# Optimization experiments

Hardware: AMD Instinct MI355X
Metric: run time of the kernel (lower is better)

Reference implementation:

```python
import jax, jax.numpy as jnp
import numpy as np
from jax import lax

B, L, D, F = 32, 512, 256, 256
K = 3
EPS = 1e-5


def _layer_norm(h, g, b):
    mu = jnp.mean(h, axis=-1, keepdims=True)
    var = jnp.var(h, axis=-1, keepdims=True)
    return (h - mu) * lax.rsqrt(var + EPS) * g + b


def _conv1d(h, w, b):
    # h: [B, L, Cin], w: [K, Cin, Cout] -> [B, L, Cout], 'same' padding (pad=1, k=3)
    return lax.conv_general_dilated(h, w, window_strides=(1,), padding=[(1, 1)],
                                    dimension_numbers=('NWC', 'WIO', 'NWC')) + b


def _duration_predictor(x, c1w, c1b, ln1g, ln1b, c2w, c2b, ln2g, ln2b, lw, lb):
    h = jax.nn.relu(_layer_norm(_conv1d(x, c1w, c1b), ln1g, ln1b))
    h = jax.nn.relu(_layer_norm(_conv1d(h, c2w, c2b), ln2g, ln2b))
    d = jax.nn.relu(h @ lw + lb)  # [B, L, 1]
    return d[..., 0]              # [B, L] (squeeze, training mode)


def _expand_one(xb, dur, M):
    # xb: [L, D], dur: [L] int. Repeat row i dur[i] times, zero-pad to M frames.
    cs = jnp.cumsum(dur)                              # [L]
    t = jnp.arange(M)                                 # [M]
    idx = jnp.searchsorted(cs, t, side='right')       # phoneme id per frame
    valid = t < cs[-1]
    out = jnp.take(xb, jnp.clip(idx, 0, xb.shape[0] - 1), axis=0)
    return jnp.where(valid[:, None], out, jnp.zeros((), xb.dtype))


def setup_inputs() -> dict:
    key = jax.random.key(0)
    ks = jax.random.split(key, 8)
    s_c = 1.0 / np.sqrt(K * F)
    s_l = 1.0 / np.sqrt(F)
    return {
        'x': jax.random.normal(ks[0], (B, L, D), jnp.float32),
        'durations': jax.random.randint(ks[1], (B, L), 0, 7),
        'mel_max_length': 4096,
        'conv1_w': jax.random.normal(ks[2], (K, D, F), jnp.float32) * s_c,
        'conv1_b': jnp.zeros((F,), jnp.float32),
        'ln1_g': jnp.ones((F,), jnp.float32),
        'ln1_b': jnp.zeros((F,), jnp.float32),
        'conv2_w': jax.random.normal(ks[3], (K, F, F), jnp.float32) * s_c,
        'conv2_b': jnp.zeros((F,), jnp.float32),
        'ln2_g': jnp.ones((F,), jnp.float32),
        'ln2_b': jnp.zeros((F,), jnp.float32),
        'lin_w': jax.random.normal(ks[4], (F, 1), jnp.float32) * s_l,
        'lin_b': jnp.zeros((1,), jnp.float32),
    }


def reference(x, durations, mel_max_length, conv1_w, conv1_b, ln1_g, ln1_b,
              conv2_w, conv2_b, ln2_g, ln2_b, lin_w, lin_b):
    dur_pred = _duration_predictor(x, conv1_w, conv1_b, ln1_g, ln1_b,
                                   conv2_w, conv2_b, ln2_g, ln2_b, lin_w, lin_b)
    dur = durations.astype(jnp.int32)
    output = jax.vmap(lambda xb, db: _expand_one(xb, db, mel_max_length))(x, dur)
    return output, dur_pred
```

## Files before the change

### kernel.cpp

```cpp
#include <hip/hip_runtime.h>

typedef __attribute__((ext_vector_type(8))) short short8;
typedef __attribute__((ext_vector_type(4))) float f32x4;

#define BATCH 32
#define LSEQ  512
#define DIN   256
#define FDIM  256
#define KTOT  768
#define MT    32
#define BK    32
#define PADA  264

__device__ __forceinline__ short f2bf(float f) {
    union { float f; unsigned u; } v; v.f = f;
    unsigned r = v.u + 0x7FFFu + ((v.u >> 16) & 1u);
    return (short)(r >> 16);
}

__global__ __launch_bounds__(512)
void prep_kernel(const int* __restrict__ dur, int* __restrict__ fidx, int M,
                 const float* __restrict__ w1, const float* __restrict__ w2,
                 short* __restrict__ wt1, short* __restrict__ wt2) {
    __shared__ int s[LSEQ];
    const int t = threadIdx.x, b = blockIdx.x;
    if (b < BATCH) {
        s[t] = dur[b * LSEQ + t];
        __syncthreads();
        for (int off = 1; off < LSEQ; off <<= 1) {
            int v = (t >= off) ? s[t - off] : 0;
            __syncthreads();
            s[t] += v;
            __syncthreads();
        }
        for (int f = t; f < M; f += 512) fidx[b * M + f] = -1;
        __syncthreads();
        int lo = (t == 0) ? 0 : s[t - 1];
        int hi = s[t];
        if (hi > M) hi = M;
        for (int j = lo; j < hi; j++) fidx[b * M + j] = b * LSEQ + t;
    } else {
        const int id = (b - BATCH) * 512 + t;
        const int n = id & 255, k = id >> 8;
        const int dst = (((k >> 5) * FDIM) + n) * BK + (k & 31);
        wt1[dst] = f2bf(w1[id]);
        wt2[dst] = f2bf(w2[id]);
    }
}

template<bool AF32, bool FUSE>
__global__ __launch_bounds__(256)
void conv_ln(const void* __restrict__ Asrc, const short* __restrict__ Bt,
             const float* __restrict__ cb, const float* __restrict__ g,
             const float* __restrict__ bta, const float* __restrict__ lw,
             const float* __restrict__ lb, short* __restrict__ Hout,
             float* __restrict__ Dout)
{
    __shared__ short As[34][PADA];
    __shared__ float redS[MT][4];
    __shared__ float redQ[MT][4];
    __shared__ float redD[MT][4];
    __shared__ float muS[MT];
    __shared__ float rsS[MT];

    const int tid  = threadIdx.x;
    const int wave = tid >> 6;
    const int lane = tid & 63;
    const int ml   = lane & 15;
    const int q    = lane >> 4;
    const int row0 = blockIdx.x * MT;
    const int bb   = row0 >> 9;
    const int r0   = row0 & (LSEQ - 1);

    for (int idx = tid; idx < 34 * 32; idx += 256) {
        const int r = idx >> 5, part = idx & 31;
        const int l2 = r0 + r - 1;
        short8 v = {0, 0, 0, 0, 0, 0, 0, 0};
        if (l2 >= 0 && l2 < LSEQ) {
            const size_t off = ((size_t)(bb * LSEQ + l2)) * DIN + part * 8;
            if (AF32) {
                const float4* s4 = (const float4*)((const float*)Asrc + off);
                float4 u0 = s4[0], u1 = s4[1];
                v[0] = f2bf(u0.x); v[1] = f2bf(u0.y); v[2] = f2bf(u0.z); v[3] = f2bf(u0.w);
                v[4] = f2bf(u1.x); v[5] = f2bf(u1.y); v[6] = f2bf(u1.z); v[7] = f2bf(u1.w);
            } else {
                v = *(const short8*)((const short*)Asrc + off);
            }
        }
        *(short8*)&As[r][part * 8] = v;
    }
    __syncthreads();

    f32x4 acc[2][4];
    #pragma unroll
    for (int mt = 0; mt < 2; mt++)
        #pragma unroll
        for (int nt = 0; nt < 4; nt++)
            #pragma unroll
            for (int r = 0; r < 4; r++)
                acc[mt][nt][r] = 0.f;

    const short* bptr = Bt + (size_t)(wave * 64 + ml) * BK + q * 8;
    #pragma unroll 1
    for (int tap = 0; tap < 3; tap++) {
        #pragma unroll
        for (int cc = 0; cc < 8; cc++) {
            short8 af0 = *(const short8*)&As[ml + tap][cc * 32 + q * 8];
            short8 af1 = *(const short8*)&As[16 + ml + tap][cc * 32 + q * 8];
            short8 b0 = *(const short8*)(bptr + 0 * 16 * BK);
            short8 b1 = *(const short8*)(bptr + 1 * 16 * BK);
            short8 b2 = *(const short8*)(bptr + 2 * 16 * BK);
            short8 b3 = *(const short8*)(bptr + 3 * 16 * BK);
            bptr += FDIM * BK;
            acc[0][0] = __builtin_amdgcn_mfma_f32_16x16x32_bf16(af0, b0, acc[0][0], 0, 0, 0);
            acc[0][1] = __builtin_amdgcn_mfma_f32_16x16x32_bf16(af0, b1, acc[0][1], 0, 0, 0);
            acc[0][2] = __builtin_amdgcn_mfma_f32_16x16x32_bf16(af0, b2, acc[0][2], 0, 0, 0);
            acc[0][3] = __builtin_amdgcn_mfma_f32_16x16x32_bf16(af0, b3, acc[0][3], 0, 0, 0);
            acc[1][0] = __builtin_amdgcn_mfma_f32_16x16x32_bf16(af1, b0, acc[1][0], 0, 0, 0);
            acc[1][1] = __builtin_amdgcn_mfma_f32_16x16x32_bf16(af1, b1, acc[1][1], 0, 0, 0);
            acc[1][2] = __builtin_amdgcn_mfma_f32_16x16x32_bf16(af1, b2, acc[1][2], 0, 0, 0);
            acc[1][3] = __builtin_amdgcn_mfma_f32_16x16x32_bf16(af1, b3, acc[1][3], 0, 0, 0);
        }
    }

    float cbv[4], gv[4], bv[4], lwv[4];
    #pragma unroll
    for (int nt = 0; nt < 4; nt++) {
        const int col = wave * 64 + nt * 16 + ml;
        cbv[nt] = cb[col]; gv[nt] = g[col]; bv[nt] = bta[col];
        lwv[nt] = FUSE ? lw[col] : 0.f;
    }
    #pragma unroll
    for (int mt = 0; mt < 2; mt++)
        #pragma unroll
        for (int nt = 0; nt < 4; nt++)
            #pragma unroll
            for (int r = 0; r < 4; r++)
                acc[mt][nt][r] += cbv[nt];

    #pragma unroll
    for (int mt = 0; mt < 2; mt++)
        #pragma unroll
        for (int r = 0; r < 4; r++) {
            float ps = 0.f, pq = 0.f;
            #pragma unroll
            for (int nt = 0; nt < 4; nt++) { float v = acc[mt][nt][r]; ps += v; pq += v * v; }
            #pragma unroll
            for (int d = 1; d < 16; d <<= 1) { ps += __shfl_xor(ps, d); pq += __shfl_xor(pq, d); }
            if (ml == 0) { const int row = mt * 16 + q * 4 + r; redS[row][wave] = ps; redQ[row][wave] = pq; }
        }
    __syncthreads();
    if (tid < MT) {
        float S = 0.f, Q = 0.f;
        #pragma unroll
        for (int w = 0; w < 4; w++) { S += redS[tid][w]; Q += redQ[tid][w]; }
        const float mu  = S * (1.f / 256.f);
        const float var = Q * (1.f / 256.f) - mu * mu;
        muS[tid] = mu; rsS[tid] = rsqrtf(var + 1e-5f);
    }
    __syncthreads();

    if (!FUSE) {
        #pragma unroll
        for (int mt = 0; mt < 2; mt++)
            #pragma unroll
            for (int r = 0; r < 4; r++) {
                const int row = mt * 16 + q * 4 + r;
                const float mu = muS[row], rs = rsS[row];
                #pragma unroll
                for (int nt = 0; nt < 4; nt++) {
                    const int col = wave * 64 + nt * 16 + ml;
                    float v = (acc[mt][nt][r] - mu) * rs * gv[nt] + bv[nt];
                    v = fmaxf(v, 0.f);
                    Hout[(size_t)(row0 + row) * FDIM + col] = f2bf(v);
                }
            }
    } else {
        #pragma unroll
        for (int mt = 0; mt < 2; mt++)
            #pragma unroll
            for (int r = 0; r < 4; r++) {
                const int row = mt * 16 + q * 4 + r;
                const float mu = muS[row], rs = rsS[row];
                float pd = 0.f;
                #pragma unroll
                for (int nt = 0; nt < 4; nt++) {
                    float v = (acc[mt][nt][r] - mu) * rs * gv[nt] + bv[nt];
                    v = fmaxf(v, 0.f);
                    pd += v * lwv[nt];
                }
                #pragma unroll
                for (int d = 1; d < 16; d <<= 1) pd += __shfl_xor(pd, d);
                if (ml == 0) redD[row][wave] = pd;
            }
        __syncthreads();
        if (tid < MT) {
            float Dv = 0.f;
            #pragma unroll
            for (int w = 0; w < 4; w++) Dv += redD[tid][w];
            Dout[row0 + tid] = fmaxf(Dv + lb[0], 0.f);
        }
    }
}

__global__ __launch_bounds__(256)
void expand_kernel(const float4* __restrict__ x4, const int* __restrict__ fidx,
                   float4* __restrict__ out4) {
    const int wave = threadIdx.x >> 6;
    const int lane = threadIdx.x & 63;
    const int fr0  = blockIdx.x * 16 + wave * 4;

    int idx[4];
    #pragma unroll
    for (int j = 0; j < 4; j++) idx[j] = fidx[fr0 + j];

    float4 v[4];
    #pragma unroll
    for (int j = 0; j < 4; j++) {
        v[j] = make_float4(0.f, 0.f, 0.f, 0.f);
        if (idx[j] >= 0) v[j] = x4[(size_t)idx[j] * 64 + lane];
    }
    #pragma unroll
    for (int j = 0; j < 4; j++)
        out4[(size_t)(fr0 + j) * 64 + lane] = v[j];
}

extern "C" void kernel_launch(void* const* d_in, const int* in_sizes, int n_in,
                              void* d_out, int out_size, void* d_ws, size_t ws_size,
                              hipStream_t stream)
{
    const float* x   = (const float*)d_in[0];
    const int*   dur = (const int*)d_in[1];
    const float* c1w = (const float*)d_in[3];
    const float* c1b = (const float*)d_in[4];
    const float* g1  = (const float*)d_in[5];
    const float* b1  = (const float*)d_in[6];
    const float* c2w = (const float*)d_in[7];
    const float* c2b = (const float*)d_in[8];
    const float* g2  = (const float*)d_in[9];
    const float* b2  = (const float*)d_in[10];
    const float* lw  = (const float*)d_in[11];
    const float* lb  = (const float*)d_in[12];

    const int M = (out_size - BATCH * LSEQ) / (BATCH * DIN);
    float* out     = (float*)d_out;
    float* dur_out = out + (size_t)BATCH * M * DIN;

    char* ws   = (char*)d_ws;
    int*  fidx = (int*)ws;
    short* wt1 = (short*)(ws + (512 << 10));
    short* wt2 = (short*)(ws + (512 << 10) + (384 << 10));
    short* h1  = (short*)(ws + (512 << 10) + 2 * (384 << 10));

    hipLaunchKernelGGL(prep_kernel, dim3(BATCH + (KTOT * FDIM) / 512), dim3(512), 0, stream,
                       dur, fidx, M, c1w, c2w, wt1, wt2);
    hipLaunchKernelGGL((conv_ln<true, false>), dim3((BATCH * LSEQ) / MT), dim3(256), 0, stream,
                       (const void*)x, wt1, c1b, g1, b1, (const float*)nullptr, (const float*)nullptr,
                       h1, (float*)nullptr);
    hipLaunchKernelGGL((conv_ln<false, true>), dim3((BATCH * LSEQ) / MT), dim3(256), 0, stream,
                       (const void*)h1, wt2, c2b, g2, b2, lw, lb,
                       (short*)nullptr, dur_out);
    hipLaunchKernelGGL(expand_kernel, dim3((BATCH * M) / 16), dim3(256), 0, stream,
                       (const float4*)x, fidx, (float4*)d_out);
}
```

Baseline: 205.5 us.

## Fuse both conv+layernorm stages into one kernel with halo recompute

Merges the two conv+LN kernels into one block-local kernel. It loads a 36-row halo of x, computes 34 rows of the first layer (including two extra halo rows via an extra accumulator set) into shared memory, then runs the second conv, LN and linear head from shared memory. This removes the bf16 intermediate round trip through global memory and one kernel launch, at the cost of a small amount of redundant compute, more LDS and more registers per block. The expand kernel also switches to nontemporal stores for the large output.

```diff
diff --git a/kernel.cpp b/kernel.cpp
--- a/kernel.cpp
+++ b/kernel.cpp
@@ -7,7 +7,6 @@
 #define LSEQ  512
 #define DIN   256
 #define FDIM  256
-#define KTOT  768
 #define MT    32
 #define BK    32
 #define PADA  264
@@ -48,20 +47,23 @@
     }
 }
 
-template<bool AF32, bool FUSE>
 __global__ __launch_bounds__(256)
-void conv_ln(const void* __restrict__ Asrc, const short* __restrict__ Bt,
-             const float* __restrict__ cb, const float* __restrict__ g,
-             const float* __restrict__ bta, const float* __restrict__ lw,
-             const float* __restrict__ lb, short* __restrict__ Hout,
-             float* __restrict__ Dout)
+void fused_dp(const float* __restrict__ x,
+              const short* __restrict__ Bt1, const short* __restrict__ Bt2,
+              const float* __restrict__ c1b, const float* __restrict__ g1v,
+              const float* __restrict__ b1v,
+              const float* __restrict__ c2b, const float* __restrict__ g2v,
+              const float* __restrict__ b2v,
+              const float* __restrict__ lw, const float* __restrict__ lb,
+              float* __restrict__ Dout)
 {
-    __shared__ short As[34][PADA];
-    __shared__ float redS[MT][4];
-    __shared__ float redQ[MT][4];
+    __shared__ short As[36][PADA];
+    __shared__ short Hs[34][PADA];
+    __shared__ float redS[34][4];
+    __shared__ float redQ[34][4];
     __shared__ float redD[MT][4];
-    __shared__ float muS[MT];
-    __shared__ float rsS[MT];
+    __shared__ float muS[34];
+    __shared__ float rsS[34];
 
     const int tid  = threadIdx.x;
     const int wave = tid >> 6;
@@ -70,28 +72,24 @@
     const int q    = lane >> 4;
     const int row0 = blockIdx.x * MT;
     const int bb   = row0 >> 9;
-    const int r0   = row0 & (LSEQ - 1);
-
-    for (int idx = tid; idx < 34 * 32; idx += 256) {
+    const int r0b  = row0 & (LSEQ - 1);
+
+    for (int idx = tid; idx < 36 * 32; idx += 256) {
         const int r = idx >> 5, part = idx & 31;
-        const int l2 = r0 + r - 1;
+        const int l2 = r0b + r - 2;
         short8 v = {0, 0, 0, 0, 0, 0, 0, 0};
         if (l2 >= 0 && l2 < LSEQ) {
-            const size_t off = ((size_t)(bb * LSEQ + l2)) * DIN + part * 8;
-            if (AF32) {
-                const float4* s4 = (const float4*)((const float*)Asrc + off);
-                float4 u0 = s4[0], u1 = s4[1];
-                v[0] = f2bf(u0.x); v[1] = f2bf(u0.y); v[2] = f2bf(u0.z); v[3] = f2bf(u0.w);
-                v[4] = f2bf(u1.x); v[5] = f2bf(u1.y); v[6] = f2bf(u1.z); v[7] = f2bf(u1.w);
-            } else {
-                v = *(const short8*)((const short*)Asrc + off);
-            }
+            const f32x4* s4 = (const f32x4*)(x + ((size_t)(bb * LSEQ + l2)) * DIN + part * 8);
+            f32x4 u0 = s4[0], u1 = s4[1];
+            v[0] = f2bf(u0.x); v[1] = f2bf(u0.y); v[2] = f2bf(u0.z); v[3] = f2bf(u0.w);
+            v[4] = f2bf(u1.x); v[5] = f2bf(u1.y); v[6] = f2bf(u1.z); v[7] = f2bf(u1.w);
         }
         *(short8*)&As[r][part * 8] = v;
     }
     __syncthreads();
 
     f32x4 acc[2][4];
+    f32x4 acce[4];
     #pragma unroll
     for (int mt = 0; mt < 2; mt++)
         #pragma unroll
@@ -99,36 +97,48 @@
             #pragma unroll
             for (int r = 0; r < 4; r++)
                 acc[mt][nt][r] = 0.f;
-
-    const short* bptr = Bt + (size_t)(wave * 64 + ml) * BK + q * 8;
-    #pragma unroll 1
-    for (int tap = 0; tap < 3; tap++) {
-        #pragma unroll
-        for (int cc = 0; cc < 8; cc++) {
-            short8 af0 = *(const short8*)&As[ml + tap][cc * 32 + q * 8];
-            short8 af1 = *(const short8*)&As[16 + ml + tap][cc * 32 + q * 8];
-            short8 b0 = *(const short8*)(bptr + 0 * 16 * BK);
-            short8 b1 = *(const short8*)(bptr + 1 * 16 * BK);
-            short8 b2 = *(const short8*)(bptr + 2 * 16 * BK);
-            short8 b3 = *(const short8*)(bptr + 3 * 16 * BK);
-            bptr += FDIM * BK;
-            acc[0][0] = __builtin_amdgcn_mfma_f32_16x16x32_bf16(af0, b0, acc[0][0], 0, 0, 0);
-            acc[0][1] = __builtin_amdgcn_mfma_f32_16x16x32_bf16(af0, b1, acc[0][1], 0, 0, 0);
-            acc[0][2] = __builtin_amdgcn_mfma_f32_16x16x32_bf16(af0, b2, acc[0][2], 0, 0, 0);
-            acc[0][3] = __builtin_amdgcn_mfma_f32_16x16x32_bf16(af0, b3, acc[0][3], 0, 0, 0);
-            acc[1][0] = __builtin_amdgcn_mfma_f32_16x16x32_bf16(af1, b0, acc[1][0], 0, 0, 0);
-            acc[1][1] = __builtin_amdgcn_mfma_f32_16x16x32_bf16(af1, b1, acc[1][1], 0, 0, 0);
-            acc[1][2] = __builtin_amdgcn_mfma_f32_16x16x32_bf16(af1, b2, acc[1][2], 0, 0, 0);
-            acc[1][3] = __builtin_amdgcn_mfma_f32_16x16x32_bf16(af1, b3, acc[1][3], 0, 0, 0);
-        }
-    }
-
-    float cbv[4], gv[4], bv[4], lwv[4];
+    #pragma unroll
+    for (int nt = 0; nt < 4; nt++)
+        #pragma unroll
+        for (int r = 0; r < 4; r++)
+            acce[nt][r] = 0.f;
+
+    {
+        const short* bptr = Bt1 + (size_t)(wave * 64 + ml) * BK + q * 8;
+        #pragma unroll 1
+        for (int tap = 0; tap < 3; tap++) {
+            int are = 32 + ml + tap; if (are > 35) are = 35;
+            #pragma unroll
+            for (int cc = 0; cc < 8; cc++) {
+                short8 af0 = *(const short8*)&As[ 0 + ml + tap][cc * 32 + q * 8];
+                short8 af1 = *(const short8*)&As[16 + ml + tap][cc * 32 + q * 8];
+                short8 af2 = *(const short8*)&As[are][cc * 32 + q * 8];
+                short8 b0 = *(const short8*)(bptr + 0 * 16 * BK);
+                short8 b1 = *(const short8*)(bptr + 1 * 16 * BK);
+                short8 b2 = *(const short8*)(bptr + 2 * 16 * BK);
+                short8 b3 = *(const short8*)(bptr + 3 * 16 * BK);
+                bptr += FDIM * BK;
+                acc[0][0] = __builtin_amdgcn_mfma_f32_16x16x32_bf16(af0, b0, acc[0][0], 0, 0, 0);
+                acc[0][1] = __builtin_amdgcn_mfma_f32_16x16x32_bf16(af0, b1, acc[0][1], 0, 0, 0);
+                acc[0][2] = __builtin_amdgcn_mfma_f32_16x16x32_bf16(af0, b2, acc[0][2], 0, 0, 0);
+                acc[0][3] = __builtin_amdgcn_mfma_f32_16x16x32_bf16(af0, b3, acc[0][3], 0, 0, 0);
+                acc[1][0] = __builtin_amdgcn_mfma_f32_16x16x32_bf16(af1, b0, acc[1][0], 0, 0, 0);
+                acc[1][1] = __builtin_amdgcn_mfma_f32_16x16x32_bf16(af1, b1, acc[1][1], 0, 0, 0);
+                acc[1][2] = __builtin_amdgcn_mfma_f32_16x16x32_bf16(af1, b2, acc[1][2], 0, 0, 0);
+                acc[1][3] = __builtin_amdgcn_mfma_f32_16x16x32_bf16(af1, b3, acc[1][3], 0, 0, 0);
+                acce[0]   = __builtin_amdgcn_mfma_f32_16x16x32_bf16(af2, b0, acce[0], 0, 0, 0);
+                acce[1]   = __builtin_amdgcn_mfma_f32_16x16x32_bf16(af2, b1, acce[1], 0, 0, 0);
+                acce[2]   = __builtin_amdgcn_mfma_f32_16x16x32_bf16(af2, b2, acce[2], 0, 0, 0);
+                acce[3]   = __builtin_amdgcn_mfma_f32_16x16x32_bf16(af2, b3, acce[3], 0, 0, 0);
+            }
+        }
+    }
+
+    float cbv[4], gv[4], bv[4];
     #pragma unroll
     for (int nt = 0; nt < 4; nt++) {
         const int col = wave * 64 + nt * 16 + ml;
-        cbv[nt] = cb[col]; gv[nt] = g[col]; bv[nt] = bta[col];
-        lwv[nt] = FUSE ? lw[col] : 0.f;
+        cbv[nt] = c1b[col]; gv[nt] = g1v[col]; bv[nt] = b1v[col];
     }
     #pragma unroll
     for (int mt = 0; mt < 2; mt++)
@@ -137,6 +147,11 @@
             #pragma unroll
             for (int r = 0; r < 4; r++)
                 acc[mt][nt][r] += cbv[nt];
+    #pragma unroll
+    for (int nt = 0; nt < 4; nt++)
+        #pragma unroll
+        for (int r = 0; r < 4; r++)
+            acce[nt][r] += cbv[nt];
 
     #pragma unroll
     for (int mt = 0; mt < 2; mt++)
@@ -149,8 +164,17 @@
             for (int d = 1; d < 16; d <<= 1) { ps += __shfl_xor(ps, d); pq += __shfl_xor(pq, d); }
             if (ml == 0) { const int row = mt * 16 + q * 4 + r; redS[row][wave] = ps; redQ[row][wave] = pq; }
         }
-    __syncthreads();
-    if (tid < MT) {
+    #pragma unroll
+    for (int r = 0; r < 2; r++) {
+        float ps = 0.f, pq = 0.f;
+        #pragma unroll
+        for (int nt = 0; nt < 4; nt++) { float v = acce[nt][r]; ps += v; pq += v * v; }
+        #pragma unroll
+        for (int d = 1; d < 16; d <<= 1) { ps += __shfl_xor(ps, d); pq += __shfl_xor(pq, d); }
+        if (ml == 0 && q == 0) { redS[32 + r][wave] = ps; redQ[32 + r][wave] = pq; }
+    }
+    __syncthreads();
+    if (tid < 34) {
         float S = 0.f, Q = 0.f;
         #pragma unroll
         for (int w = 0; w < 4; w++) { S += redS[tid][w]; Q += redQ[tid][w]; }
@@ -160,52 +184,136 @@
     }
     __syncthreads();
 
-    if (!FUSE) {
-        #pragma unroll
-        for (int mt = 0; mt < 2; mt++)
-            #pragma unroll
-            for (int r = 0; r < 4; r++) {
-                const int row = mt * 16 + q * 4 + r;
-                const float mu = muS[row], rs = rsS[row];
-                #pragma unroll
-                for (int nt = 0; nt < 4; nt++) {
-                    const int col = wave * 64 + nt * 16 + ml;
-                    float v = (acc[mt][nt][r] - mu) * rs * gv[nt] + bv[nt];
-                    v = fmaxf(v, 0.f);
-                    Hout[(size_t)(row0 + row) * FDIM + col] = f2bf(v);
-                }
-            }
-    } else {
-        #pragma unroll
-        for (int mt = 0; mt < 2; mt++)
-            #pragma unroll
-            for (int r = 0; r < 4; r++) {
-                const int row = mt * 16 + q * 4 + r;
-                const float mu = muS[row], rs = rsS[row];
-                float pd = 0.f;
-                #pragma unroll
-                for (int nt = 0; nt < 4; nt++) {
-                    float v = (acc[mt][nt][r] - mu) * rs * gv[nt] + bv[nt];
-                    v = fmaxf(v, 0.f);
-                    pd += v * lwv[nt];
-                }
-                #pragma unroll
-                for (int d = 1; d < 16; d <<= 1) pd += __shfl_xor(pd, d);
-                if (ml == 0) redD[row][wave] = pd;
-            }
-        __syncthreads();
-        if (tid < MT) {
-            float Dv = 0.f;
-            #pragma unroll
-            for (int w = 0; w < 4; w++) Dv += redD[tid][w];
-            Dout[row0 + tid] = fmaxf(Dv + lb[0], 0.f);
-        }
+    #pragma unroll
+    for (int mt = 0; mt < 2; mt++)
+        #pragma unroll
+        for (int r = 0; r < 4; r++) {
+            const int row = mt * 16 + q * 4 + r;
+            const bool ok = (unsigned)(r0b - 1 + row) < (unsigned)LSEQ;
+            const float mu = muS[row], rs = rsS[row];
+            #pragma unroll
+            for (int nt = 0; nt < 4; nt++) {
+                const int col = wave * 64 + nt * 16 + ml;
+                float v = (acc[mt][nt][r] - mu) * rs * gv[nt] + bv[nt];
+                v = ok ? fmaxf(v, 0.f) : 0.f;
+                Hs[row][col] = f2bf(v);
+            }
+        }
+    if (q == 0) {
+        #pragma unroll
+        for (int r = 0; r < 2; r++) {
+            const int row = 32 + r;
+            const bool ok = (unsigned)(r0b - 1 + row) < (unsigned)LSEQ;
+            const float mu = muS[row], rs = rsS[row];
+            #pragma unroll
+            for (int nt = 0; nt < 4; nt++) {
+                const int col = wave * 64 + nt * 16 + ml;
+                float v = (acce[nt][r] - mu) * rs * gv[nt] + bv[nt];
+                v = ok ? fmaxf(v, 0.f) : 0.f;
+                Hs[row][col] = f2bf(v);
+            }
+        }
+    }
+    __syncthreads();
+
+    f32x4 acc2[2][4];
+    #pragma unroll
+    for (int mt = 0; mt < 2; mt++)
+        #pragma unroll
+        for (int nt = 0; nt < 4; nt++)
+            #pragma unroll
+            for (int r = 0; r < 4; r++)
+                acc2[mt][nt][r] = 0.f;
+    {
+        const short* bptr = Bt2 + (size_t)(wave * 64 + ml) * BK + q * 8;
+        #pragma unroll 1
+        for (int tap = 0; tap < 3; tap++) {
+            #pragma unroll
+            for (int cc = 0; cc < 8; cc++) {
+                short8 af0 = *(const short8*)&Hs[ 0 + ml + tap][cc * 32 + q * 8];
+                short8 af1 = *(const short8*)&Hs[16 + ml + tap][cc * 32 + q * 8];
+                short8 b0 = *(const short8*)(bptr + 0 * 16 * BK);
+                short8 b1 = *(const short8*)(bptr + 1 * 16 * BK);
+                short8 b2 = *(const short8*)(bptr + 2 * 16 * BK);
+                short8 b3 = *(const short8*)(bptr + 3 * 16 * BK);
+                bptr += FDIM * BK;
+                acc2[0][0] = __builtin_amdgcn_mfma_f32_16x16x32_bf16(af0, b0, acc2[0][0], 0, 0, 0);
+                acc2[0][1] = __builtin_amdgcn_mfma_f32_16x16x32_bf16(af0, b1, acc2[0][1], 0, 0, 0);
+                acc2[0][2] = __builtin_amdgcn_mfma_f32_16x16x32_bf16(af0, b2, acc2[0][2], 0, 0, 0);
+                acc2[0][3] = __builtin_amdgcn_mfma_f32_16x16x32_bf16(af0, b3, acc2[0][3], 0, 0, 0);
+                acc2[1][0] = __builtin_amdgcn_mfma_f32_16x16x32_bf16(af1, b0, acc2[1][0], 0, 0, 0);
+                acc2[1][1] = __builtin_amdgcn_mfma_f32_16x16x32_bf16(af1, b1, acc2[1][1], 0, 0, 0);
+                acc2[1][2] = __builtin_amdgcn_mfma_f32_16x16x32_bf16(af1, b2, acc2[1][2], 0, 0, 0);
+                acc2[1][3] = __builtin_amdgcn_mfma_f32_16x16x32_bf16(af1, b3, acc2[1][3], 0, 0, 0);
+            }
+        }
+    }
+
+    float lwv[4];
+    #pragma unroll
+    for (int nt = 0; nt < 4; nt++) {
+        const int col = wave * 64 + nt * 16 + ml;
+        cbv[nt] = c2b[col]; gv[nt] = g2v[col]; bv[nt] = b2v[col]; lwv[nt] = lw[col];
+    }
+    #pragma unroll
+    for (int mt = 0; mt < 2; mt++)
+        #pragma unroll
+        for (int nt = 0; nt < 4; nt++)
+            #pragma unroll
+            for (int r = 0; r < 4; r++)
+                acc2[mt][nt][r] += cbv[nt];
+
+    #pragma unroll
+    for (int mt = 0; mt < 2; mt++)
+        #pragma unroll
+        for (int r = 0; r < 4; r++) {
+            float ps = 0.f, pq = 0.f;
+            #pragma unroll
+            for (int nt = 0; nt < 4; nt++) { float v = acc2[mt][nt][r]; ps += v; pq += v * v; }
+            #pragma unroll
+            for (int d = 1; d < 16; d <<= 1) { ps += __shfl_xor(ps, d); pq += __shfl_xor(pq, d); }
+            if (ml == 0) { const int row = mt * 16 + q * 4 + r; redS[row][wave] = ps; redQ[row][wave] = pq; }
+        }
+    __syncthreads();
+    if (tid < MT) {
+        float S = 0.f, Q = 0.f;
+        #pragma unroll
+        for (int w = 0; w < 4; w++) { S += redS[tid][w]; Q += redQ[tid][w]; }
+        const float mu  = S * (1.f / 256.f);
+        const float var = Q * (1.f / 256.f) - mu * mu;
+        muS[tid] = mu; rsS[tid] = rsqrtf(var + 1e-5f);
+    }
+    __syncthreads();
+
+    #pragma unroll
+    for (int mt = 0; mt < 2; mt++)
+        #pragma unroll
+        for (int r = 0; r < 4; r++) {
+            const int row = mt * 16 + q * 4 + r;
+            const float mu = muS[row], rs = rsS[row];
+            float pd = 0.f;
+            #pragma unroll
+            for (int nt = 0; nt < 4; nt++) {
+                float v = (acc2[mt][nt][r] - mu) * rs * gv[nt] + bv[nt];
+                v = fmaxf(v, 0.f);
+                pd += v * lwv[nt];
+            }
+            #pragma unroll
+            for (int d = 1; d < 16; d <<= 1) pd += __shfl_xor(pd, d);
+            if (ml == 0) redD[row][wave] = pd;
+        }
+    __syncthreads();
+    if (tid < MT) {
+        float Dv = 0.f;
+        #pragma unroll
+        for (int w = 0; w < 4; w++) Dv += redD[tid][w];
+        Dout[row0 + tid] = fmaxf(Dv + lb[0], 0.f);
     }
 }
 
 __global__ __launch_bounds__(256)
-void expand_kernel(const float4* __restrict__ x4, const int* __restrict__ fidx,
-                   float4* __restrict__ out4) {
+void expand_kernel(const f32x4* __restrict__ x4, const int* __restrict__ fidx,
+                   f32x4* __restrict__ out4) {
     const int wave = threadIdx.x >> 6;
     const int lane = threadIdx.x & 63;
     const int fr0  = blockIdx.x * 16 + wave * 4;
@@ -214,15 +322,15 @@
     #pragma unroll
     for (int j = 0; j < 4; j++) idx[j] = fidx[fr0 + j];
 
-    float4 v[4];
+    f32x4 v[4];
     #pragma unroll
     for (int j = 0; j < 4; j++) {
-        v[j] = make_float4(0.f, 0.f, 0.f, 0.f);
+        v[j] = (f32x4){0.f, 0.f, 0.f, 0.f};
         if (idx[j] >= 0) v[j] = x4[(size_t)idx[j] * 64 + lane];
     }
     #pragma unroll
     for (int j = 0; j < 4; j++)
-        out4[(size_t)(fr0 + j) * 64 + lane] = v[j];
+        __builtin_nontemporal_store(v[j], &out4[(size_t)(fr0 + j) * 64 + lane]);
 }
 
 extern "C" void kernel_launch(void* const* d_in, const int* in_sizes, int n_in,
@@ -250,16 +358,11 @@
     int*  fidx = (int*)ws;
     short* wt1 = (short*)(ws + (512 << 10));
     short* wt2 = (short*)(ws + (512 << 10) + (384 << 10));
-    short* h1  = (short*)(ws + (512 << 10) + 2 * (384 << 10));
-
-    hipLaunchKernelGGL(prep_kernel, dim3(BATCH + (KTOT * FDIM) / 512), dim3(512), 0, stream,
+
+    hipLaunchKernelGGL(prep_kernel, dim3(BATCH + (3 * DIN * FDIM) / 512), dim3(512), 0, stream,
                        dur, fidx, M, c1w, c2w, wt1, wt2);
-    hipLaunchKernelGGL((conv_ln<true, false>), dim3((BATCH * LSEQ) / MT), dim3(256), 0, stream,
-                       (const void*)x, wt1, c1b, g1, b1, (const float*)nullptr, (const float*)nullptr,
-                       h1, (float*)nullptr);
-    hipLaunchKernelGGL((conv_ln<false, true>), dim3((BATCH * LSEQ) / MT), dim3(256), 0, stream,
-                       (const void*)h1, wt2, c2b, g2, b2, lw, lb,
-                       (short*)nullptr, dur_out);
+    hipLaunchKernelGGL(fused_dp, dim3((BATCH * LSEQ) / MT), dim3(256), 0, stream,
+                       x, wt1, wt2, c1b, g1, b1, c2b, g2, b2, lw, lb, dur_out);
     hipLaunchKernelGGL(expand_kernel, dim3((BATCH * M) / 16), dim3(256), 0, stream,
-                       (const float4*)x, fidx, (float4*)d_out);
-}
+                       (const f32x4*)x, fidx, (f32x4*)d_out);
+}
```

Result: slower. 210.9 us (+2.6%).
